# Optimization experiments

Hardware: AMD Instinct MI355X
Metric: run time of the kernel (lower is better)

Reference implementation:

```python
import jax, jax.numpy as jnp
import numpy as np

IN_F, OUT_F, LAT, RES, K, B = 512, 512, 512, 64, 3, 8
EPS = 1e-08
C_LIN = 1.0 / np.sqrt(LAT)          # EqualizedWeight scale for linear
C_CONV = 1.0 / np.sqrt(IN_F * K * K)  # EqualizedWeight scale for conv


def setup_inputs() -> dict:
    key = jax.random.key(0)
    k1, k2, k3, k4 = jax.random.split(key, 4)
    return {
        "x": jax.random.normal(k1, (B, IN_F, RES, RES), dtype=jnp.float32),
        "latent": jax.random.normal(k2, (B, LAT), dtype=jnp.float32),
        "w_lin": jax.random.normal(k3, (IN_F, LAT), dtype=jnp.float32),
        "b_lin": jnp.ones((IN_F,), dtype=jnp.float32),
        "w_conv": jax.random.normal(k4, (OUT_F, IN_F, K, K), dtype=jnp.float32),
        "b_conv": jnp.zeros((OUT_F,), dtype=jnp.float32),
    }


def reference(x, latent, w_lin, b_lin, w_conv, b_conv):
    # EqualizedLinear: s = latent @ (w_lin*c).T + b_lin*lr_mul  -> [B, IN_F]
    s = latent @ (w_lin * C_LIN).T + b_lin
    # ModulatedConv2d. Per-sample weight w[b,o,i,k,k] = (w_conv*c)[o,i,k,k]*s[b,i],
    # demodulated by sigma_inv[b,o] = rsqrt(sum_{i,k,k} w^2 + eps).
    w = w_conv * C_CONV  # [O, I, K, K]
    # sum_{k,k} w^2 over spatial -> [O, I], then contract with s^2 -> [B, O]
    w2 = jnp.sum(w * w, axis=(2, 3))  # [O, I]
    sigma_inv = jax.lax.rsqrt(jnp.einsum('oi,bi->bo', w2, s * s) + EPS)
    # conv(x, w*s_b) == conv(x * s_b, w): modulate input, single batched conv,
    # then demodulate output per (b, o). Avoids materializing B*O filters.
    x_mod = x * s[:, :, None, None]
    y = jax.lax.conv_general_dilated(
        x_mod, w,
        window_strides=(1, 1),
        padding=[((K - 1) // 2, (K - 1) // 2)] * 2,
        dimension_numbers=('NCHW', 'OIHW', 'NCHW'),
    )
    y = y * sigma_inv[:, :, None, None] + b_conv[None, :, None, None]
    return y
```

## Files before the change

### kernel.cpp

```cpp
#include <hip/hip_runtime.h>
#include <hip/hip_bf16.h>

#define IN_F 512
#define OUT_F 512
#define LATD 512
#define RES 64
#define BATCH 8
#define EPSV 1e-8f

static constexpr float C_LIN  = 0.04419417382415922f;
static constexpr float C_CONV = 0.014731391274719739f;

typedef __attribute__((ext_vector_type(8)))  short short8;
typedef __attribute__((ext_vector_type(16))) float f32x16;

union BF { __hip_bfloat16 h; short s; };

__device__ __forceinline__ void async_load16(const char* g, char* l) {
  __builtin_amdgcn_global_load_lds(
      (const __attribute__((address_space(1))) unsigned int*)g,
      (__attribute__((address_space(3))) unsigned int*)l, 16, 0, 0);
}

__global__ void k_prep(const float* __restrict__ w_conv,
                       short* __restrict__ wb,
                       float* __restrict__ w2,
                       char* __restrict__ xmp,
                       const float* __restrict__ latent,
                       const float* __restrict__ w_lin,
                       const float* __restrict__ b_lin,
                       float* __restrict__ s) {
  const int t = blockIdx.x * 256 + threadIdx.x;
  {
    const int o = t >> 9;
    const int i = t & 511;
    const float* src = w_conv + (size_t)t * 9;
    const int c = i >> 4, hf0 = (i >> 3) & 1, ch = i & 7;
    const int ob = o >> 7, ol = o & 127;
    short* dst = wb + (size_t)(c * 4 + ob) * 18432 + hf0 * 1024 + ol * 8 + ch;
    float sum = 0.f;
#pragma unroll
    for (int tap = 0; tap < 9; ++tap) {
      const float v = src[tap] * C_CONV;
      sum += v * v;
      BF cv; cv.h = __float2bfloat16(v);
      dst[tap * 2048] = cv.s;
    }
    w2[t] = sum;
  }

  if (blockIdx.x < 256) {
    char* base = xmp + (size_t)blockIdx.x * 139392;
    for (int q = threadIdx.x; q < 520; q += 256) {
      int h, hf, w;
      if (q < 132)      { h = 0;  hf = (q >= 66) ? 1 : 0; w = q - hf * 66; }
      else if (q < 264) { const int r = q - 132; h = 65; hf = (r >= 66) ? 1 : 0; w = r - hf * 66; }
      else              { const int r = q - 264; h = (r >> 2) + 1; hf = (r >> 1) & 1; w = (r & 1) * 65; }
      *(uint4*)(base + ((size_t)(h * 132 + hf * 66 + w)) * 16) = make_uint4(0u, 0u, 0u, 0u);
    }
  }

  if (blockIdx.x < 128) {
    const int wv = threadIdx.x >> 6, lane = threadIdx.x & 63;
    const int i = blockIdx.x * 4 + wv;
    const float4* wl = (const float4*)(w_lin + (size_t)i * LATD);
    const float4 w0 = wl[lane * 2], w1 = wl[lane * 2 + 1];
    float acc[BATCH];
#pragma unroll
    for (int b = 0; b < BATCH; ++b) {
      const float4* lt = (const float4*)(latent + (size_t)b * LATD);
      const float4 l0 = lt[lane * 2], l1 = lt[lane * 2 + 1];
      acc[b] = w0.x * l0.x + w0.y * l0.y + w0.z * l0.z + w0.w * l0.w +
               w1.x * l1.x + w1.y * l1.y + w1.z * l1.z + w1.w * l1.w;
    }
#pragma unroll
    for (int b = 0; b < BATCH; ++b) {
      float v = acc[b];
#pragma unroll
      for (int off = 32; off > 0; off >>= 1) v += __shfl_down(v, off);
      if (lane == 0) s[b * IN_F + i] = v * C_LIN + b_lin[i];
    }
  }
}

__global__ void k_mod_sigma(const float* __restrict__ x,
                            const float* __restrict__ s,
                            char* __restrict__ xmp,
                            const float* __restrict__ w2,
                            float* __restrict__ sigma_inv) {
  if (blockIdx.x < 128) {
    const int o = blockIdx.x * 4 + (threadIdx.x >> 6);
    const int lane = threadIdx.x & 63;
    float acc[BATCH];
#pragma unroll
    for (int b = 0; b < BATCH; ++b) acc[b] = 0.f;
#pragma unroll
    for (int k = 0; k < 8; ++k) {
      const int i = k * 64 + lane;
      const float w = w2[o * IN_F + i];
#pragma unroll
      for (int b = 0; b < BATCH; ++b) {
        const float sv = s[b * IN_F + i];
        acc[b] += w * sv * sv;
      }
    }
#pragma unroll
    for (int b = 0; b < BATCH; ++b) {
      float v = acc[b];
#pragma unroll
      for (int off = 32; off > 0; off >>= 1) v += __shfl_down(v, off);
      if (lane == 0) sigma_inv[b * OUT_F + o] = rsqrtf(v + EPSV);
    }
    return;
  }
  const int bid  = blockIdx.x - 128;
  const int h8   = bid & 7;
  const int ic32 = (bid >> 3) & 15;
  const int b    = bid >> 7;
  __shared__ float tile[32][65];
  const int tid = threadIdx.x;
  const int il = tid >> 3, w8 = (tid & 7) * 8;
  const int i  = ic32 * 32 + il;
  const float sv = s[b * IN_F + i];
  const float* xrow = x + (size_t)(b * IN_F + i) * (RES * RES) + w8;
  const int w = tid >> 2, part = tid & 3;
  const int chalf = part >> 1, hf = part & 1;
  const int c = ic32 * 2 + chalf;
  char* dstb = xmp + (size_t)(c * 8 + b) * 139392 + ((size_t)hf * 66 + (w + 1)) * 16;

  float4 v0 = *(const float4*)(xrow + (size_t)(h8 * 8) * RES);
  float4 v1 = *(const float4*)(xrow + (size_t)(h8 * 8) * RES + 4);
#pragma unroll
  for (int hh = 0; hh < 8; ++hh) {
    const int h = h8 * 8 + hh;
    tile[il][w8 + 0] = v0.x * sv; tile[il][w8 + 1] = v0.y * sv;
    tile[il][w8 + 2] = v0.z * sv; tile[il][w8 + 3] = v0.w * sv;
    tile[il][w8 + 4] = v1.x * sv; tile[il][w8 + 5] = v1.y * sv;
    tile[il][w8 + 6] = v1.z * sv; tile[il][w8 + 7] = v1.w * sv;
    float4 n0, n1;
    if (hh < 7) {
      n0 = *(const float4*)(xrow + (size_t)(h + 1) * RES);
      n1 = *(const float4*)(xrow + (size_t)(h + 1) * RES + 4);
    }
    __syncthreads();
    short8 pk;
#pragma unroll
    for (int j = 0; j < 8; ++j) {
      BF cv; cv.h = __float2bfloat16(tile[chalf * 16 + hf * 8 + j][w]);
      pk[j] = cv.s;
    }
    *(short8*)(dstb + (size_t)(h + 1) * 2112) = pk;
    __syncthreads();
    v0 = n0; v1 = n1;
  }
}

__global__ __launch_bounds__(512, 2)
void k_conv(const char* __restrict__ xmp,
            const short* __restrict__ wbg,
            const float* __restrict__ sigma_inv,
            const float* __restrict__ b_conv,
            float* __restrict__ out) {
  __shared__ __align__(16) char lds[115968];
  const int l = blockIdx.x;
  const int ob = (l >> 3) & 3;
  const int b  = l & 7;
  const int h0 = (l >> 5) * 8;
  const int o0 = ob * 128;
  const int tid = threadIdx.x;
  const int wave = tid >> 6, lane = tid & 63;
  const int l31 = lane & 31, half = lane >> 5;
  const int oh = wave >> 2;
  const int q  = wave & 3;
  const int r0 = (q >> 1) * 4;
  const int c0 = (q & 1) * 32;
  const int st = (wave >> 2) & 1;
  const int dseq[3] = {st, st + 1, st ? 0 : 2};

  f32x16 acc[2][4];
#pragma unroll
  for (int i = 0; i < 2; ++i)
#pragma unroll
    for (int j = 0; j < 4; ++j)
#pragma unroll
      for (int r = 0; r < 16; ++r) acc[i][j][r] = 0.f;

  const char* xsrc0 = xmp + (size_t)b * 139392 + (size_t)h0 * 2112;
  const char* wsrc0 = (const char*)wbg + (size_t)ob * 36864;

#pragma unroll
  for (int k = 0; k < 2; ++k) {
    const int j = tid + k * 512;
    async_load16(xsrc0 + j * 16, lds + j * 16);
  }
  if (tid < 296) { const int j = 1024 + tid; async_load16(xsrc0 + j * 16, lds + j * 16); }
#pragma unroll
  for (int k = 0; k < 4; ++k) {
    const int j = tid + k * 512;
    async_load16(wsrc0 + j * 16, lds + 42240 + j * 16);
  }
  if (tid < 256) { const int j = 2048 + tid; async_load16(wsrc0 + j * 16, lds + 42240 + j * 16); }
  __syncthreads();

  for (int ic = 0; ic < 32; ++ic) {
    const int p = ic & 1;
    if (ic + 1 < 32) {
      const char* xs  = xsrc0 + (size_t)(ic + 1) * (8 * 139392);
      const char* wsr = wsrc0 + (size_t)(ic + 1) * 147456;
      char* xd = lds + (p ^ 1) * 21120;
      char* wd = lds + 42240 + (p ^ 1) * 36864;
#pragma unroll
      for (int k = 0; k < 2; ++k) {
        const int j = tid + k * 512;
        async_load16(xs + j * 16, xd + j * 16);
      }
      if (tid < 296) { const int j = 1024 + tid; async_load16(xs + j * 16, xd + j * 16); }
#pragma unroll
      for (int k = 0; k < 4; ++k) {
        const int j = tid + k * 512;
        async_load16(wsr + j * 16, wd + j * 16);
      }
      if (tid < 256) { const int j = 2048 + tid; async_load16(wsr + j * 16, wd + j * 16); }
    }
    const char* xp = lds + p * 21120;
    const char* wp = lds + 42240 + p * 36864;

    short8 a_cur[2], a_nxt[2];
#pragma unroll
    for (int f = 0; f < 2; ++f)
      a_cur[f] = *(const short8*)(
          wp + dseq[0] * 4096 + half * 2048 + (oh * 64 + f * 32 + l31) * 16);

#pragma unroll
    for (int dwi = 0; dwi < 3; ++dwi) {
      const int dw = dseq[dwi];
      short8 brow[6];
#pragma unroll
      for (int rr = 0; rr < 6; ++rr)
        brow[rr] = *(const short8*)(
            xp + (((r0 + rr) * 132) + half * 66 + c0 + dw + l31) * 16);
#pragma unroll
      for (int dh = 0; dh < 3; ++dh) {
        if (!(dwi == 2 && dh == 2)) {
          const int dh_n = (dh < 2) ? dh + 1 : 0;
          const int dw_n = (dh < 2) ? dw : dseq[dwi + 1];
#pragma unroll
          for (int f = 0; f < 2; ++f)
            a_nxt[f] = *(const short8*)(
                wp + (dh_n * 3 + dw_n) * 4096 + half * 2048 + (oh * 64 + f * 32 + l31) * 16);
        }
        __builtin_amdgcn_s_setprio(1);
#pragma unroll
        for (int tpr = 0; tpr < 4; ++tpr)
#pragma unroll
          for (int f = 0; f < 2; ++f)
            acc[f][tpr] = __builtin_amdgcn_mfma_f32_32x32x16_bf16(
                a_cur[f], brow[tpr + dh], acc[f][tpr], 0, 0, 0);
        __builtin_amdgcn_s_setprio(0);
        a_cur[0] = a_nxt[0]; a_cur[1] = a_nxt[1];
      }
    }
    __syncthreads();
  }

#pragma unroll
  for (int f = 0; f < 2; ++f) {
#pragma unroll
    for (int g = 0; g < 4; ++g) {
#pragma unroll
      for (int r = 0; r < 4; ++r) {
        const int o = o0 + oh * 64 + f * 32 + r + 8 * g + 4 * half;
        const float sig  = sigma_inv[b * OUT_F + o];
        const float bias = b_conv[o];
        const int reg = g * 4 + r;
#pragma unroll
        for (int tpr = 0; tpr < 4; ++tpr) {
          const int h = h0 + r0 + tpr;
          const int w = c0 + l31;
          out[(((size_t)(b * OUT_F + o) * RES + h) * RES) + w] =
              acc[f][tpr][reg] * sig + bias;
        }
      }
    }
  }
}

extern "C" void kernel_launch(void* const* d_in, const int* in_sizes, int n_in,
                              void* d_out, int out_size, void* d_ws, size_t ws_size,
                              hipStream_t stream) {
  const float* x      = (const float*)d_in[0];
  const float* latent = (const float*)d_in[1];
  const float* w_lin  = (const float*)d_in[2];
  const float* b_lin  = (const float*)d_in[3];
  const float* w_conv = (const float*)d_in[4];
  const float* b_conv = (const float*)d_in[5];
  float* out = (float*)d_out;

  char* ws = (char*)d_ws;
  char*  xmp       = ws;
  short* wb        = (short*)(ws + 35684352);
  float* w2        = (float*)(ws + 40402944);
  float* s         = (float*)(ws + 41451520);
  float* sigma_inv = (float*)(ws + 41467904);

  k_prep<<<1024, 256, 0, stream>>>(w_conv, wb, w2, xmp, latent, w_lin, b_lin, s);
  k_mod_sigma<<<128 + 1024, 256, 0, stream>>>(x, s, xmp, w2, sigma_inv);
  k_conv<<<256, 512, 0, stream>>>(xmp, wb, sigma_inv, b_conv, out);
}
```

Measured before the change: 246.7 us.

## Load activation rows directly from global into registers instead of LDS staging

Removes the LDS double buffer for the input activation tile. Each wave now reads its B-operand rows straight from global memory into registers, prefetching the next kernel-column rows between MFMA groups. Only the weight tiles stay staged in LDS, which cuts LDS use from about 113KB to 72KB and may allow more blocks per CU. The cost is exposed global-load latency on the MFMA critical path and repeated global reads of overlapping rows across waves, relying on cache hits.

```diff
diff --git a/kernel.cpp b/kernel.cpp
--- a/kernel.cpp
+++ b/kernel.cpp
@@ -161,7 +161,7 @@
             const float* __restrict__ sigma_inv,
             const float* __restrict__ b_conv,
             float* __restrict__ out) {
-  __shared__ __align__(16) char lds[115968];
+  __shared__ __align__(16) char lds[73728];
   const int l = blockIdx.x;
   const int ob = (l >> 3) & 3;
   const int b  = l & 7;
@@ -185,36 +185,33 @@
 #pragma unroll
       for (int r = 0; r < 16; ++r) acc[i][j][r] = 0.f;
 
-  const char* xsrc0 = xmp + (size_t)b * 139392 + (size_t)h0 * 2112;
   const char* wsrc0 = (const char*)wbg + (size_t)ob * 36864;
 
-#pragma unroll
-  for (int k = 0; k < 2; ++k) {
-    const int j = tid + k * 512;
-    async_load16(xsrc0 + j * 16, lds + j * 16);
-  }
-  if (tid < 296) { const int j = 1024 + tid; async_load16(xsrc0 + j * 16, lds + j * 16); }
+  const char* xr[6];
+#pragma unroll
+  for (int rr = 0; rr < 6; ++rr)
+    xr[rr] = xmp + (size_t)b * 139392 +
+             (size_t)((h0 + r0 + rr) * 132 + half * 66 + c0 + l31) * 16;
+
 #pragma unroll
   for (int k = 0; k < 4; ++k) {
     const int j = tid + k * 512;
-    async_load16(wsrc0 + j * 16, lds + 42240 + j * 16);
-  }
-  if (tid < 256) { const int j = 2048 + tid; async_load16(wsrc0 + j * 16, lds + 42240 + j * 16); }
+    async_load16(wsrc0 + j * 16, lds + j * 16);
+  }
+  if (tid < 256) { const int j = 2048 + tid; async_load16(wsrc0 + j * 16, lds + j * 16); }
+
+  short8 brow[6];
+#pragma unroll
+  for (int rr = 0; rr < 6; ++rr)
+    brow[rr] = *(const short8*)(xr[rr] + dseq[0] * 16);
   __syncthreads();
 
   for (int ic = 0; ic < 32; ++ic) {
     const int p = ic & 1;
+    const char* wp = lds + p * 36864;
     if (ic + 1 < 32) {
-      const char* xs  = xsrc0 + (size_t)(ic + 1) * (8 * 139392);
       const char* wsr = wsrc0 + (size_t)(ic + 1) * 147456;
-      char* xd = lds + (p ^ 1) * 21120;
-      char* wd = lds + 42240 + (p ^ 1) * 36864;
-#pragma unroll
-      for (int k = 0; k < 2; ++k) {
-        const int j = tid + k * 512;
-        async_load16(xs + j * 16, xd + j * 16);
-      }
-      if (tid < 296) { const int j = 1024 + tid; async_load16(xs + j * 16, xd + j * 16); }
+      char* wd = lds + (p ^ 1) * 36864;
 #pragma unroll
       for (int k = 0; k < 4; ++k) {
         const int j = tid + k * 512;
@@ -222,8 +219,6 @@
       }
       if (tid < 256) { const int j = 2048 + tid; async_load16(wsr + j * 16, wd + j * 16); }
     }
-    const char* xp = lds + p * 21120;
-    const char* wp = lds + 42240 + p * 36864;
 
     short8 a_cur[2], a_nxt[2];
 #pragma unroll
@@ -234,11 +229,6 @@
 #pragma unroll
     for (int dwi = 0; dwi < 3; ++dwi) {
       const int dw = dseq[dwi];
-      short8 brow[6];
-#pragma unroll
-      for (int rr = 0; rr < 6; ++rr)
-        brow[rr] = *(const short8*)(
-            xp + (((r0 + rr) * 132) + half * 66 + c0 + dw + l31) * 16);
 #pragma unroll
       for (int dh = 0; dh < 3; ++dh) {
         if (!(dwi == 2 && dh == 2)) {
@@ -258,7 +248,23 @@
                 a_cur[f], brow[tpr + dh], acc[f][tpr], 0, 0, 0);
         __builtin_amdgcn_s_setprio(0);
         a_cur[0] = a_nxt[0]; a_cur[1] = a_nxt[1];
-      }
+        if (dwi < 2 && dh < 2)
+          brow[dh] = *(const short8*)(xr[dh] + dseq[dwi + 1] * 16);
+      }
+      if (dwi < 2) {
+        const int dwn = dseq[dwi + 1];
+#pragma unroll
+        for (int rr = 2; rr < 6; ++rr)
+          brow[rr] = *(const short8*)(xr[rr] + dwn * 16);
+      }
+    }
+
+#pragma unroll
+    for (int rr = 0; rr < 6; ++rr) xr[rr] += 8 * 139392;
+    if (ic + 1 < 32) {
+#pragma unroll
+      for (int rr = 0; rr < 6; ++rr)
+        brow[rr] = *(const short8*)(xr[rr] + dseq[0] * 16);
     }
     __syncthreads();
   }
```

Measured after the change: 266.4 us. 1.08x slower.
